# Optimization experiments

Measured on AMD Instinct MI355X. Metric: run time of the kernel, lower is better.

The kernel has to match this reference:

```python
import jax, jax.numpy as jnp
import numpy as np


def setup_inputs() -> dict:
    key = jax.random.key(0)
    ks = jax.random.split(key, 6)
    B, C, H, W = 16, 256, 128, 128
    r = C // 16
    inp = {}
    inp["x"] = jax.random.normal(ks[0], (B, C, H, W), jnp.float32)
    # DCA channel-MLP (1x1 convs acting on pooled [B,C,1,1] maps)
    inp["w1"] = jax.random.normal(ks[1], (r, C), jnp.float32) * 0.05
    inp["b1"] = jnp.zeros((r,), jnp.float32)
    inp["w2"] = jax.random.normal(ks[2], (C, r), jnp.float32) * 0.05
    inp["b2"] = jnp.zeros((C,), jnp.float32)
    # DSA offset conv 2->18, k=3 pad=1 (small offsets keep sampling sane)
    inp["off_w"] = jax.random.normal(ks[3], (18, 2, 3, 3), jnp.float32) * 0.05
    inp["off_b"] = jnp.zeros((18,), jnp.float32)
    # DeformConv 2->1, k=3 pad=1
    inp["dc_w"] = jax.random.normal(ks[4], (1, 2, 3, 3), jnp.float32) * 0.2
    inp["dc_b"] = jnp.zeros((1,), jnp.float32)
    # BatchNorm2d(1) in eval mode (running stats at init)
    inp["bn_gamma"] = jnp.ones((1,), jnp.float32)
    inp["bn_beta"] = jnp.zeros((1,), jnp.float32)
    inp["bn_mean"] = jnp.zeros((1,), jnp.float32)
    inp["bn_var"] = jnp.ones((1,), jnp.float32)
    return inp


def _deform_conv3x3(cat, offsets, dc_w, dc_b):
    # cat: [B,2,H,W], offsets: [B,18,H,W] ordered as (dy,dx) per kernel tap
    B, Cin, H, W = cat.shape
    K = 9
    off = offsets.reshape(B, K, 2, H, W)
    ky = (jnp.arange(K) // 3 - 1).astype(cat.dtype)[None, :, None, None]
    kx = (jnp.arange(K) % 3 - 1).astype(cat.dtype)[None, :, None, None]
    ii = jnp.arange(H, dtype=cat.dtype)[None, None, :, None]
    jj = jnp.arange(W, dtype=cat.dtype)[None, None, None, :]
    py = ii + ky + off[:, :, 0]  # [B,K,H,W]
    px = jj + kx + off[:, :, 1]
    y0 = jnp.floor(py)
    x0 = jnp.floor(px)
    wy = py - y0
    wx = px - x0
    y0i = y0.astype(jnp.int32)
    x0i = x0.astype(jnp.int32)
    catl = jnp.transpose(cat, (0, 2, 3, 1))  # [B,H,W,Cin]
    bidx = jnp.arange(B)[:, None, None, None]

    def corner(yi, xi):
        valid = ((yi >= 0) & (yi < H) & (xi >= 0) & (xi < W)).astype(cat.dtype)
        v = catl[bidx, jnp.clip(yi, 0, H - 1), jnp.clip(xi, 0, W - 1)]  # [B,K,H,W,Cin]
        return v * valid[..., None]

    v00 = corner(y0i, x0i)
    v01 = corner(y0i, x0i + 1)
    v10 = corner(y0i + 1, x0i)
    v11 = corner(y0i + 1, x0i + 1)
    wy_ = wy[..., None]
    wx_ = wx[..., None]
    samp = (v00 * (1 - wy_) * (1 - wx_) + v01 * (1 - wy_) * wx_
            + v10 * wy_ * (1 - wx_) + v11 * wy_ * wx_)  # [B,K,H,W,Cin]
    w = dc_w.reshape(dc_w.shape[0], Cin, K)  # [O,Cin,K]
    out = jnp.einsum('bkhwc,ock->bohw', samp, w) + dc_b[None, :, None, None]
    return out  # [B,1,H,W]


def reference(x, w1, b1, w2, b2, off_w, off_b, dc_w, dc_b,
              bn_gamma, bn_beta, bn_mean, bn_var):
    # ---- DCA: channel attention ----
    def mlp(v):  # v: [B,C]
        h = jax.nn.relu(v @ w1.T + b1)
        return h @ w2.T + b2

    avg = x.mean((2, 3))
    mx = x.max((2, 3))
    wch = jax.nn.sigmoid(mlp(avg) + mlp(mx))[:, :, None, None]
    y = x * wch
    # ---- DSA: deformable spatial attention ----
    avgmap = y.mean(1, keepdims=True)
    maxmap = y.max(1, keepdims=True)
    cat = jnp.concatenate([maxmap, avgmap], axis=1)  # [B,2,H,W]
    offsets = jax.lax.conv_general_dilated(
        cat, off_w, (1, 1), 'SAME',
        dimension_numbers=('NCHW', 'OIHW', 'NCHW')) + off_b[None, :, None, None]
    d = _deform_conv3x3(cat, offsets, dc_w, dc_b)
    inv = bn_gamma[None, :, None, None] / jnp.sqrt(bn_var[None, :, None, None] + 1e-5)
    d = (d - bn_mean[None, :, None, None]) * inv + bn_beta[None, :, None, None]
    ws = jax.nn.sigmoid(d)
    # residual (in_channels == out_channels, residual=True)
    return y * ws + x
```

## Files before the change

### kernel.cpp

```cpp
#include <hip/hip_runtime.h>
#include <math.h>

#define BB 16
#define CC 256
#define HH 128
#define WW 128
#define HWSZ 16384
#define RR 16

__global__ void pool_kernel(const float* __restrict__ x,
                            float* __restrict__ avg_out,
                            float* __restrict__ max_out) {
    int bc = blockIdx.x;
    const float4* xp = reinterpret_cast<const float4*>(x + (size_t)bc * HWSZ);
    int tid = threadIdx.x;
    float s = 0.f, m = -INFINITY;
#pragma unroll
    for (int it = 0; it < 16; ++it) {
        float4 v = xp[tid + it * 256];
        s += v.x + v.y + v.z + v.w;
        m = fmaxf(m, fmaxf(fmaxf(v.x, v.y), fmaxf(v.z, v.w)));
    }
    for (int o = 32; o > 0; o >>= 1) {
        s += __shfl_down(s, o);
        m = fmaxf(m, __shfl_down(m, o));
    }
    __shared__ float ss[4], sm[4];
    int wave = tid >> 6;
    if ((tid & 63) == 0) { ss[wave] = s; sm[wave] = m; }
    __syncthreads();
    if (tid == 0) {
        float st = ss[0] + ss[1] + ss[2] + ss[3];
        float mt = fmaxf(fmaxf(sm[0], sm[1]), fmaxf(sm[2], sm[3]));
        avg_out[bc] = st * (1.0f / HWSZ);
        max_out[bc] = mt;
    }
}

__global__ void mlp_kernel(const float* __restrict__ avg, const float* __restrict__ mx,
                           const float* __restrict__ w1, const float* __restrict__ b1,
                           const float* __restrict__ w2, const float* __restrict__ b2,
                           float* __restrict__ wch) {
    int b = blockIdx.x;
    int tid = threadIdx.x;
    __shared__ float s_in[2][CC];
    __shared__ float s_h[2][RR];
    s_in[0][tid] = avg[b * CC + tid];
    s_in[1][tid] = mx[b * CC + tid];
    __syncthreads();
    int pair = tid >> 3;
    int lane8 = tid & 7;
    int which = pair >> 4;
    int row = pair & 15;
    float acc = 0.f;
#pragma unroll
    for (int c0 = 0; c0 < CC; c0 += 8)
        acc += s_in[which][c0 + lane8] * w1[row * CC + c0 + lane8];
    acc += __shfl_down(acc, 4);
    acc += __shfl_down(acc, 2);
    acc += __shfl_down(acc, 1);
    if (lane8 == 0) s_h[which][row] = fmaxf(acc + b1[row], 0.f);
    __syncthreads();
    float o = 2.f * b2[tid];
#pragma unroll
    for (int r = 0; r < RR; ++r)
        o += w2[tid * RR + r] * (s_h[0][r] + s_h[1][r]);
    wch[b * CC + tid] = 1.f / (1.f + expf(-o));
}

__global__ void spatial_stats_kernel(const float* __restrict__ x,
                                     const float* __restrict__ wch,
                                     float* __restrict__ cat) {
    int blk = blockIdx.x;
    int b = blk >> 4;
    int chunk = blk & 15;
    int tid = threadIdx.x;
    __shared__ float s_w[CC];
    s_w[tid] = wch[b * CC + tid];
    __syncthreads();
    int p4 = chunk * 256 + tid;
    const float4* xp = reinterpret_cast<const float4*>(x) + (size_t)b * CC * (HWSZ / 4) + p4;
    float sx = 0.f, sy = 0.f, sz = 0.f, sw = 0.f;
    float mx_ = -INFINITY, my_ = -INFINITY, mz_ = -INFINITY, mw_ = -INFINITY;
#pragma unroll 4
    for (int c = 0; c < CC; ++c) {
        float4 v = xp[(size_t)c * (HWSZ / 4)];
        float w = s_w[c];
        float vx = v.x * w, vy = v.y * w, vz = v.z * w, vw = v.w * w;
        sx += vx; sy += vy; sz += vz; sw += vw;
        mx_ = fmaxf(mx_, vx); my_ = fmaxf(my_, vy);
        mz_ = fmaxf(mz_, vz); mw_ = fmaxf(mw_, vw);
    }
    const float inv = 1.f / CC;
    float4 m = {mx_, my_, mz_, mw_};
    float4 a = {sx * inv, sy * inv, sz * inv, sw * inv};
    float4* catp = reinterpret_cast<float4*>(cat);
    catp[((size_t)b * 2 + 0) * (HWSZ / 4) + p4] = m;
    catp[((size_t)b * 2 + 1) * (HWSZ / 4) + p4] = a;
}

__global__ __launch_bounds__(256) void dsa_kernel(
    const float* __restrict__ cat,
    const float* __restrict__ off_w, const float* __restrict__ off_b,
    const float* __restrict__ dc_w, const float* __restrict__ dc_b,
    const float* __restrict__ bn_gamma, const float* __restrict__ bn_beta,
    const float* __restrict__ bn_mean, const float* __restrict__ bn_var,
    float* __restrict__ wsout) {
    __shared__ float s_offw[324], s_offb[18], s_dcw[18];
    __shared__ float s_bnscale, s_bnshift, s_dcb;
    int tid = threadIdx.x;
    for (int idx = tid; idx < 324; idx += 256) s_offw[idx] = off_w[idx];
    if (tid < 18) { s_offb[tid] = off_b[tid]; s_dcw[tid] = dc_w[tid]; }
    if (tid == 0) {
        float inv = bn_gamma[0] * rsqrtf(bn_var[0] + 1e-5f);
        s_bnscale = inv;
        s_bnshift = bn_beta[0] - bn_mean[0] * inv;
        s_dcb = dc_b[0];
    }
    __syncthreads();
    int blk = blockIdx.x;
    int b = blk >> 6;
    int p = (blk & 63) * 256 + tid;
    int i = p >> 7, j = p & 127;
    const float* c0 = cat + ((size_t)b * 2 + 0) * HWSZ;
    const float* c1 = cat + ((size_t)b * 2 + 1) * HWSZ;
    float n0[9], n1[9];
#pragma unroll
    for (int ky = 0; ky < 3; ++ky)
#pragma unroll
        for (int kx = 0; kx < 3; ++kx) {
            int yy = i + ky - 1, xx = j + kx - 1;
            bool v = (yy >= 0) && (yy < HH) && (xx >= 0) && (xx < WW);
            int idx = yy * WW + xx;
            n0[ky * 3 + kx] = v ? c0[idx] : 0.f;
            n1[ky * 3 + kx] = v ? c1[idx] : 0.f;
        }
    float off[18];
#pragma unroll
    for (int k = 0; k < 18; ++k) {
        float acc = s_offb[k];
#pragma unroll
        for (int t = 0; t < 9; ++t)
            acc += n0[t] * s_offw[(k * 2 + 0) * 9 + t] + n1[t] * s_offw[(k * 2 + 1) * 9 + t];
        off[k] = acc;
    }
    float d = s_dcb;
#pragma unroll
    for (int k = 0; k < 9; ++k) {
        float py = (float)i + (float)(k / 3 - 1) + off[2 * k];
        float px = (float)j + (float)(k % 3 - 1) + off[2 * k + 1];
        float y0f = floorf(py), x0f = floorf(px);
        float wy = py - y0f, wx = px - x0f;
        int y0 = (int)y0f, x0 = (int)x0f;
        float w00 = (1.f - wy) * (1.f - wx), w01 = (1.f - wy) * wx;
        float w10 = wy * (1.f - wx), w11 = wy * wx;
        float s0 = 0.f, s1 = 0.f;
#pragma unroll
        for (int cy = 0; cy < 2; ++cy)
#pragma unroll
            for (int cx = 0; cx < 2; ++cx) {
                int yi = y0 + cy, xi = x0 + cx;
                bool v = (yi >= 0) && (yi < HH) && (xi >= 0) && (xi < WW);
                float ww = (cy == 0) ? (cx == 0 ? w00 : w01) : (cx == 0 ? w10 : w11);
                if (v) {
                    int idx = yi * WW + xi;
                    s0 += c0[idx] * ww;
                    s1 += c1[idx] * ww;
                }
            }
        d += s0 * s_dcw[k] + s1 * s_dcw[9 + k];
    }
    d = d * s_bnscale + s_bnshift;
    wsout[(size_t)b * HWSZ + p] = 1.f / (1.f + expf(-d));
}

__global__ void final_kernel(const float* __restrict__ x, const float* __restrict__ wch,
                             const float* __restrict__ wsmap, float* __restrict__ out) {
    size_t t = (size_t)blockIdx.x * 256 + threadIdx.x;
    int plane = (int)(t >> 12);
    int b = plane >> 8;
    int c = plane & 255;
    int p4 = (int)(t & 4095);
    float4 xv = reinterpret_cast<const float4*>(x)[t];
    float4 wv = reinterpret_cast<const float4*>(wsmap)[(size_t)b * 4096 + p4];
    float wc = wch[b * 256 + c];
    float4 o;
    o.x = xv.x * (1.f + wc * wv.x);
    o.y = xv.y * (1.f + wc * wv.y);
    o.z = xv.z * (1.f + wc * wv.z);
    o.w = xv.w * (1.f + wc * wv.w);
    reinterpret_cast<float4*>(out)[t] = o;
}

extern "C" void kernel_launch(void* const* d_in, const int* in_sizes, int n_in,
                              void* d_out, int out_size, void* d_ws, size_t ws_size,
                              hipStream_t stream) {
    const float* x       = (const float*)d_in[0];
    const float* w1      = (const float*)d_in[1];
    const float* b1      = (const float*)d_in[2];
    const float* w2      = (const float*)d_in[3];
    const float* b2      = (const float*)d_in[4];
    const float* off_w   = (const float*)d_in[5];
    const float* off_b   = (const float*)d_in[6];
    const float* dc_w    = (const float*)d_in[7];
    const float* dc_b    = (const float*)d_in[8];
    const float* bn_gamma= (const float*)d_in[9];
    const float* bn_beta = (const float*)d_in[10];
    const float* bn_mean = (const float*)d_in[11];
    const float* bn_var  = (const float*)d_in[12];

    float* wsf   = (float*)d_ws;
    float* avg   = wsf;
    float* mx    = wsf + 4096;
    float* wch   = wsf + 8192;
    float* cat   = wsf + 12288;
    float* wsmap = wsf + 12288 + 524288;
    float* out   = (float*)d_out;

    pool_kernel<<<BB * CC, 256, 0, stream>>>(x, avg, mx);
    mlp_kernel<<<BB, 256, 0, stream>>>(avg, mx, w1, b1, w2, b2, wch);
    spatial_stats_kernel<<<256, 256, 0, stream>>>(x, wch, cat);
    dsa_kernel<<<1024, 256, 0, stream>>>(cat, off_w, off_b, dc_w, dc_b,
                                         bn_gamma, bn_beta, bn_mean, bn_var, wsmap);
    final_kernel<<<65536, 256, 0, stream>>>(x, wch, wsmap, out);
}
```

Before: 578.7 us.

## Split channel loop across waves in spatial stats and fold MLP into it

Result: no change. 568.9 us (-1.7%).

```diff
diff --git a/kernel.cpp b/kernel.cpp
--- a/kernel.cpp
+++ b/kernel.cpp
@@ -37,66 +37,89 @@
     }
 }
 
-__global__ void mlp_kernel(const float* __restrict__ avg, const float* __restrict__ mx,
-                           const float* __restrict__ w1, const float* __restrict__ b1,
-                           const float* __restrict__ w2, const float* __restrict__ b2,
-                           float* __restrict__ wch) {
-    int b = blockIdx.x;
+__global__ __launch_bounds__(256) void spatial_stats_kernel(
+    const float* __restrict__ x,
+    const float* __restrict__ avg, const float* __restrict__ mxin,
+    const float* __restrict__ w1, const float* __restrict__ b1,
+    const float* __restrict__ w2, const float* __restrict__ b2,
+    float* __restrict__ cat) {
+    int blk = blockIdx.x;
+    int b = blk >> 6;
+    int chunk = blk & 63;
     int tid = threadIdx.x;
     __shared__ float s_in[2][CC];
     __shared__ float s_h[2][RR];
+    __shared__ float s_w[CC];
+    __shared__ float s_red[4][8][64];
     s_in[0][tid] = avg[b * CC + tid];
-    s_in[1][tid] = mx[b * CC + tid];
-    __syncthreads();
-    int pair = tid >> 3;
-    int lane8 = tid & 7;
-    int which = pair >> 4;
-    int row = pair & 15;
-    float acc = 0.f;
-#pragma unroll
-    for (int c0 = 0; c0 < CC; c0 += 8)
-        acc += s_in[which][c0 + lane8] * w1[row * CC + c0 + lane8];
-    acc += __shfl_down(acc, 4);
-    acc += __shfl_down(acc, 2);
-    acc += __shfl_down(acc, 1);
-    if (lane8 == 0) s_h[which][row] = fmaxf(acc + b1[row], 0.f);
-    __syncthreads();
-    float o = 2.f * b2[tid];
-#pragma unroll
-    for (int r = 0; r < RR; ++r)
-        o += w2[tid * RR + r] * (s_h[0][r] + s_h[1][r]);
-    wch[b * CC + tid] = 1.f / (1.f + expf(-o));
-}
-
-__global__ void spatial_stats_kernel(const float* __restrict__ x,
-                                     const float* __restrict__ wch,
-                                     float* __restrict__ cat) {
-    int blk = blockIdx.x;
-    int b = blk >> 4;
-    int chunk = blk & 15;
-    int tid = threadIdx.x;
-    __shared__ float s_w[CC];
-    s_w[tid] = wch[b * CC + tid];
-    __syncthreads();
-    int p4 = chunk * 256 + tid;
-    const float4* xp = reinterpret_cast<const float4*>(x) + (size_t)b * CC * (HWSZ / 4) + p4;
+    s_in[1][tid] = mxin[b * CC + tid];
+    __syncthreads();
+    {
+        int pair = tid >> 3;
+        int lane8 = tid & 7;
+        int which = pair >> 4;
+        int row = pair & 15;
+        float acc = 0.f;
+#pragma unroll
+        for (int c0 = 0; c0 < CC; c0 += 8)
+            acc += s_in[which][c0 + lane8] * w1[row * CC + c0 + lane8];
+        acc += __shfl_down(acc, 4);
+        acc += __shfl_down(acc, 2);
+        acc += __shfl_down(acc, 1);
+        if (lane8 == 0) s_h[which][row] = fmaxf(acc + b1[row], 0.f);
+    }
+    __syncthreads();
+    {
+        float o = 2.f * b2[tid];
+#pragma unroll
+        for (int r = 0; r < RR; ++r)
+            o += w2[tid * RR + r] * (s_h[0][r] + s_h[1][r]);
+        s_w[tid] = 1.f / (1.f + expf(-o));
+    }
+    __syncthreads();
+    int pp = tid & 63;
+    int csplit = tid >> 6;
+    int p4 = chunk * 64 + pp;
+    const float4* xp = reinterpret_cast<const float4*>(x)
+                       + (size_t)b * CC * (HWSZ / 4)
+                       + (size_t)csplit * 64 * (HWSZ / 4) + p4;
     float sx = 0.f, sy = 0.f, sz = 0.f, sw = 0.f;
     float mx_ = -INFINITY, my_ = -INFINITY, mz_ = -INFINITY, mw_ = -INFINITY;
-#pragma unroll 4
-    for (int c = 0; c < CC; ++c) {
-        float4 v = xp[(size_t)c * (HWSZ / 4)];
-        float w = s_w[c];
-        float vx = v.x * w, vy = v.y * w, vz = v.z * w, vw = v.w * w;
-        sx += vx; sy += vy; sz += vz; sw += vw;
-        mx_ = fmaxf(mx_, vx); my_ = fmaxf(my_, vy);
-        mz_ = fmaxf(mz_, vz); mw_ = fmaxf(mw_, vw);
-    }
-    const float inv = 1.f / CC;
-    float4 m = {mx_, my_, mz_, mw_};
-    float4 a = {sx * inv, sy * inv, sz * inv, sw * inv};
-    float4* catp = reinterpret_cast<float4*>(cat);
-    catp[((size_t)b * 2 + 0) * (HWSZ / 4) + p4] = m;
-    catp[((size_t)b * 2 + 1) * (HWSZ / 4) + p4] = a;
+    for (int cb = 0; cb < 8; ++cb) {
+        float4 v[8];
+#pragma unroll
+        for (int u = 0; u < 8; ++u)
+            v[u] = xp[(size_t)(cb * 8 + u) * (HWSZ / 4)];
+#pragma unroll
+        for (int u = 0; u < 8; ++u) {
+            float w = s_w[csplit * 64 + cb * 8 + u];
+            float vx = v[u].x * w, vy = v[u].y * w, vz = v[u].z * w, vw = v[u].w * w;
+            sx += vx; sy += vy; sz += vz; sw += vw;
+            mx_ = fmaxf(mx_, vx); my_ = fmaxf(my_, vy);
+            mz_ = fmaxf(mz_, vz); mw_ = fmaxf(mw_, vw);
+        }
+    }
+    s_red[csplit][0][pp] = sx; s_red[csplit][1][pp] = sy;
+    s_red[csplit][2][pp] = sz; s_red[csplit][3][pp] = sw;
+    s_red[csplit][4][pp] = mx_; s_red[csplit][5][pp] = my_;
+    s_red[csplit][6][pp] = mz_; s_red[csplit][7][pp] = mw_;
+    __syncthreads();
+    if (csplit == 0) {
+        float fs[4], fm[4];
+#pragma unroll
+        for (int e = 0; e < 4; ++e)
+            fs[e] = s_red[0][e][pp] + s_red[1][e][pp] + s_red[2][e][pp] + s_red[3][e][pp];
+#pragma unroll
+        for (int e = 0; e < 4; ++e)
+            fm[e] = fmaxf(fmaxf(s_red[0][e + 4][pp], s_red[1][e + 4][pp]),
+                          fmaxf(s_red[2][e + 4][pp], s_red[3][e + 4][pp]));
+        const float inv = 1.f / CC;
+        float4 m = {fm[0], fm[1], fm[2], fm[3]};
+        float4 a = {fs[0] * inv, fs[1] * inv, fs[2] * inv, fs[3] * inv};
+        float4* catp = reinterpret_cast<float4*>(cat);
+        catp[((size_t)b * 2 + 0) * (HWSZ / 4) + p4] = m;
+        catp[((size_t)b * 2 + 1) * (HWSZ / 4) + p4] = a;
+    }
 }
 
 __global__ __launch_bounds__(256) void dsa_kernel(
@@ -130,10 +153,11 @@
 #pragma unroll
         for (int kx = 0; kx < 3; ++kx) {
             int yy = i + ky - 1, xx = j + kx - 1;
-            bool v = (yy >= 0) && (yy < HH) && (xx >= 0) && (xx < WW);
-            int idx = yy * WW + xx;
-            n0[ky * 3 + kx] = v ? c0[idx] : 0.f;
-            n1[ky * 3 + kx] = v ? c1[idx] : 0.f;
+            float v = ((yy >= 0) & (yy < HH) & (xx >= 0) & (xx < WW)) ? 1.f : 0.f;
+            int yc = min(max(yy, 0), HH - 1), xc = min(max(xx, 0), WW - 1);
+            int idx = yc * WW + xc;
+            n0[ky * 3 + kx] = c0[idx] * v;
+            n1[ky * 3 + kx] = c1[idx] * v;
         }
     float off[18];
 #pragma unroll
@@ -152,21 +176,20 @@
         float y0f = floorf(py), x0f = floorf(px);
         float wy = py - y0f, wx = px - x0f;
         int y0 = (int)y0f, x0 = (int)x0f;
-        float w00 = (1.f - wy) * (1.f - wx), w01 = (1.f - wy) * wx;
-        float w10 = wy * (1.f - wx), w11 = wy * wx;
         float s0 = 0.f, s1 = 0.f;
 #pragma unroll
         for (int cy = 0; cy < 2; ++cy)
 #pragma unroll
             for (int cx = 0; cx < 2; ++cx) {
                 int yi = y0 + cy, xi = x0 + cx;
-                bool v = (yi >= 0) && (yi < HH) && (xi >= 0) && (xi < WW);
-                float ww = (cy == 0) ? (cx == 0 ? w00 : w01) : (cx == 0 ? w10 : w11);
-                if (v) {
-                    int idx = yi * WW + xi;
-                    s0 += c0[idx] * ww;
-                    s1 += c1[idx] * ww;
-                }
+                float valid = ((yi >= 0) & (yi < HH) & (xi >= 0) & (xi < WW)) ? 1.f : 0.f;
+                float wwy = cy ? wy : (1.f - wy);
+                float wwx = cx ? wx : (1.f - wx);
+                float ww = wwy * wwx * valid;
+                int yc = min(max(yi, 0), HH - 1), xc = min(max(xi, 0), WW - 1);
+                int idx = yc * WW + xc;
+                s0 += c0[idx] * ww;
+                s1 += c1[idx] * ww;
             }
         d += s0 * s_dcw[k] + s1 * s_dcw[9 + k];
     }
@@ -192,6 +215,37 @@
     reinterpret_cast<float4*>(out)[t] = o;
 }
 
+__global__ void mlp_kernel(const float* __restrict__ avg, const float* __restrict__ mx,
+                           const float* __restrict__ w1, const float* __restrict__ b1,
+                           const float* __restrict__ w2, const float* __restrict__ b2,
+                           float* __restrict__ wch) {
+    int b = blockIdx.x;
+    int tid = threadIdx.x;
+    __shared__ float s_in[2][CC];
+    __shared__ float s_h[2][RR];
+    s_in[0][tid] = avg[b * CC + tid];
+    s_in[1][tid] = mx[b * CC + tid];
+    __syncthreads();
+    int pair = tid >> 3;
+    int lane8 = tid & 7;
+    int which = pair >> 4;
+    int row = pair & 15;
+    float acc = 0.f;
+#pragma unroll
+    for (int c0 = 0; c0 < CC; c0 += 8)
+        acc += s_in[which][c0 + lane8] * w1[row * CC + c0 + lane8];
+    acc += __shfl_down(acc, 4);
+    acc += __shfl_down(acc, 2);
+    acc += __shfl_down(acc, 1);
+    if (lane8 == 0) s_h[which][row] = fmaxf(acc + b1[row], 0.f);
+    __syncthreads();
+    float o = 2.f * b2[tid];
+#pragma unroll
+    for (int r = 0; r < RR; ++r)
+        o += w2[tid * RR + r] * (s_h[0][r] + s_h[1][r]);
+    wch[b * CC + tid] = 1.f / (1.f + expf(-o));
+}
+
 extern "C" void kernel_launch(void* const* d_in, const int* in_sizes, int n_in,
                               void* d_out, int out_size, void* d_ws, size_t ws_size,
                               hipStream_t stream) {
@@ -219,7 +273,7 @@
 
     pool_kernel<<<BB * CC, 256, 0, stream>>>(x, avg, mx);
     mlp_kernel<<<BB, 256, 0, stream>>>(avg, mx, w1, b1, w2, b2, wch);
-    spatial_stats_kernel<<<256, 256, 0, stream>>>(x, wch, cat);
+    spatial_stats_kernel<<<1024, 256, 0, stream>>>(x, avg, mx, w1, b1, w2, b2, cat);
     dsa_kernel<<<1024, 256, 0, stream>>>(cat, off_w, off_b, dc_w, dc_b,
                                          bn_gamma, bn_beta, bn_mean, bn_var, wsmap);
     final_kernel<<<65536, 256, 0, stream>>>(x, wch, wsmap, out);
```
